# Optimization experiments

Measured on AMD Instinct MI355X. Metric: run time of the kernel, lower is better.

## Reference

```python
import jax, jax.numpy as jnp
import numpy as np
import math

B, LQ, LKV = 8, 1024, 1024
EQ, EKV, H, HD = 1024, 768, 8, 128

def setup_inputs() -> dict:
    key = jax.random.key(0)
    ks = jax.random.split(key, 8)
    def xavier(k, shape, fan_in, fan_out):
        a = math.sqrt(6.0 / (fan_in + fan_out))
        return jax.random.uniform(k, shape, jnp.float32, -a, a)
    return {
        "query": jax.random.normal(ks[0], (B, LQ, EQ), jnp.float32),
        "key": jax.random.normal(ks[1], (B, LKV, EKV), jnp.float32),
        "value": jax.random.normal(ks[2], (B, LKV, EKV), jnp.float32),
        "w_q": xavier(ks[3], (H, EQ, HD), EQ, HD),
        "w_k": xavier(ks[4], (H, EKV, HD), EKV, HD),
        "w_v": xavier(ks[5], (H, EKV, HD), EKV, HD),
        "proj_w": xavier(ks[6], (EQ, H * HD), H * HD, EQ),
        "proj_b": jnp.zeros((EQ,), jnp.float32),
    }

def reference(query, key, value, w_q, w_k, w_v, proj_w, proj_b):
    hd = w_q.shape[-1]
    # per-head projections: [H, B, L, hd]
    q = jnp.einsum('ble,hed->hbld', query, w_q)
    k = jnp.einsum('ble,hed->hbld', key, w_k)
    v = jnp.einsum('ble,hed->hbld', value, w_v)
    # scaled dot-product scores [H, B, Lq, Lkv]
    score = jnp.einsum('hbld,hbmd->hblm', q, k) / jnp.sqrt(jnp.asarray(hd, q.dtype))
    attn = jax.nn.softmax(score, axis=-1)
    out = jnp.einsum('hblm,hbmd->hbld', attn, v)
    # concat heads along feature dim: [B, Lq, H*hd] (head h -> slice h*hd:(h+1)*hd)
    Bsz, Lq = query.shape[0], query.shape[1]
    out = jnp.transpose(out, (1, 2, 0, 3)).reshape(Bsz, Lq, -1)
    out = out @ proj_w.T + proj_b  # dropout is identity at eval
    # torch returns attention_weights as [H*B, Lq, Lkv]
    attn_flat = attn.reshape(-1, attn.shape[-2], attn.shape[-1])
    return out, attn_flat
```

## Files before the change

### kernel.cpp

```cpp
#include <hip/hip_runtime.h>
#include <math.h>


using bf16x8 = __attribute__((ext_vector_type(8))) short;
using f32x4  = __attribute__((ext_vector_type(4))) float;

__device__ __forceinline__ unsigned bf16_rne(float x) {
    unsigned u = __float_as_uint(x);
    return (u + 0x7fffu + ((u >> 16) & 1u)) >> 16;
}

#define AS1 __attribute__((address_space(1)))
#define AS3 __attribute__((address_space(3)))

__device__ __forceinline__ void gl_lds16(const short* g, short* l) {
    __builtin_amdgcn_global_load_lds((AS1 unsigned*)g, (AS3 unsigned*)l, 16, 0, 0);
}

__global__ __launch_bounds__(256) void split_f32(
    const float* __restrict__ src, short* __restrict__ hi,
    short* __restrict__ lo)
{
    const long i = ((long)blockIdx.x * 256 + threadIdx.x) * 8;
    const float4 a = *(const float4*)(src + i);
    const float4 b = *(const float4*)(src + i + 4);
    const float fv[8] = {a.x, a.y, a.z, a.w, b.x, b.y, b.z, b.w};
    bf16x8 h, l;
    #pragma unroll
    for (int j = 0; j < 8; ++j) {
        unsigned hb = bf16_rne(fv[j]);
        h[j] = (short)hb;
        l[j] = (short)bf16_rne(fv[j] - __uint_as_float(hb << 16));
    }
    *(bf16x8*)(hi + i) = h;
    *(bf16x8*)(lo + i) = l;
}

__global__ __launch_bounds__(256) void transpose_split(
    const float* __restrict__ src, short* __restrict__ dhi,
    short* __restrict__ dlo, int R, int C)
{
    __shared__ float tile[32][33];
    src += (long)blockIdx.z * R * C;
    dhi += (long)blockIdx.z * R * C;
    dlo += (long)blockIdx.z * R * C;
    const int r0 = blockIdx.y * 32, c0 = blockIdx.x * 32;
    const int tx = threadIdx.x & 31, ty = threadIdx.x >> 5;
    #pragma unroll
    for (int i = 0; i < 4; ++i)
        tile[ty + i * 8][tx] = src[(long)(r0 + ty + i * 8) * C + c0 + tx];
    __syncthreads();
    #pragma unroll
    for (int i = 0; i < 4; ++i) {
        const float v = tile[tx][ty + i * 8];
        const unsigned h = bf16_rne(v);
        const long o = (long)(c0 + ty + i * 8) * R + r0 + tx;
        dhi[o] = (short)h;
        dlo[o] = (short)bf16_rne(v - __uint_as_float(h << 16));
    }
}

template <bool AF32, int EP, bool BIAS>
__global__ __launch_bounds__(256, 2) void gemm_bb(
    const void* __restrict__ A0, const void* __restrict__ A1, int lda, long aHS, long aBS,
    const short* __restrict__ B0, const short* __restrict__ B1, int ldb, long bHS, long bBS,
    void* __restrict__ C0, void* __restrict__ C1, int ldc, long cHS, long cBS,
    int K, float scale, const float* __restrict__ bias)
{
    const int z = blockIdx.z, hh = z >> 3, bb = z & 7;
    const long aoff = (long)hh * aHS + (long)bb * aBS;
    const long boff = (long)hh * bHS + (long)bb * bBS;
    const long coff = (long)hh * cHS + (long)bb * cBS;

    __shared__ short lAhi[4096];
    __shared__ short lAlo[4096];
    __shared__ short lBhi[4096];
    __shared__ short lBlo[4096];

    const int t    = threadIdx.x;
    const int lane = t & 63, wid = t >> 6;
    const int wr = wid >> 1, wc = wid & 1;
    const int fr = lane & 15, fg = lane >> 4;

    const int m0 = blockIdx.y * 128, n0 = blockIdx.x * 128;

    const short* Bh = B0 + boff;
    const short* Bl = B1 + boff;
    const short* Ah = AF32 ? nullptr : (const short*)A0 + aoff;
    const short* Al = AF32 ? nullptr : (const short*)A1 + aoff;
    const float* Af = AF32 ? (const float*)A0 + aoff : nullptr;

    const int glrow = (lane >> 2);
    const int glk   = (lane & 3) * 8;
    const int srow = t >> 1;
    const int shalf = (t & 1) * 16;

    f32x4 acc[4][4] = {};

    for (int k0 = 0; k0 < K; k0 += 32) {
        if (AF32) {
            const float* g = Af + (long)(m0 + srow) * lda + k0 + shalf;
            const float4 f0 = *(const float4*)(g);
            const float4 f1 = *(const float4*)(g + 4);
            const float4 f2 = *(const float4*)(g + 8);
            const float4 f3 = *(const float4*)(g + 12);
            const float fv[16] = {f0.x, f0.y, f0.z, f0.w, f1.x, f1.y, f1.z, f1.w,
                                  f2.x, f2.y, f2.z, f2.w, f3.x, f3.y, f3.z, f3.w};
            bf16x8 h0, l0, h1, l1;
            #pragma unroll
            for (int i = 0; i < 8; ++i) {
                unsigned ha = bf16_rne(fv[i]);
                h0[i] = (short)ha;
                l0[i] = (short)bf16_rne(fv[i] - __uint_as_float(ha << 16));
                unsigned hb = bf16_rne(fv[8 + i]);
                h1[i] = (short)hb;
                l1[i] = (short)bf16_rne(fv[8 + i] - __uint_as_float(hb << 16));
            }
            const int sb = srow * 32 + shalf;
            *(bf16x8*)&lAhi[sb] = h0;  *(bf16x8*)&lAhi[sb + 8] = h1;
            *(bf16x8*)&lAlo[sb] = l0;  *(bf16x8*)&lAlo[sb + 8] = l1;
        } else {
            #pragma unroll
            for (int j = 0; j < 2; ++j) {
                const int rowb = wid * 32 + j * 16 + glrow;
                const long go = (long)(m0 + rowb) * lda + k0 + glk;
                gl_lds16(Ah + go, &lAhi[(wid * 2 + j) * 512]);
                gl_lds16(Al + go, &lAlo[(wid * 2 + j) * 512]);
            }
        }
        #pragma unroll
        for (int j = 0; j < 2; ++j) {
            const int rowb = wid * 32 + j * 16 + glrow;
            const long go = (long)(n0 + rowb) * ldb + k0 + glk;
            gl_lds16(Bh + go, &lBhi[(wid * 2 + j) * 512]);
            gl_lds16(Bl + go, &lBlo[(wid * 2 + j) * 512]);
        }
        __syncthreads();

        bf16x8 va[4], wa[4];
        #pragma unroll
        for (int m = 0; m < 4; ++m) {
            const int off = (wr * 64 + m * 16 + fr) * 32 + fg * 8;
            va[m] = *(const bf16x8*)&lAhi[off];
            wa[m] = *(const bf16x8*)&lAlo[off];
        }
        #pragma unroll
        for (int n = 0; n < 4; ++n) {
            const int off = (wc * 64 + n * 16 + fr) * 32 + fg * 8;
            const bf16x8 vb = *(const bf16x8*)&lBhi[off];
            const bf16x8 wb = *(const bf16x8*)&lBlo[off];
            #pragma unroll
            for (int m = 0; m < 4; ++m) {
                acc[m][n] = __builtin_amdgcn_mfma_f32_16x16x32_bf16(va[m], vb, acc[m][n], 0, 0, 0);
                acc[m][n] = __builtin_amdgcn_mfma_f32_16x16x32_bf16(va[m], wb, acc[m][n], 0, 0, 0);
                acc[m][n] = __builtin_amdgcn_mfma_f32_16x16x32_bf16(wa[m], vb, acc[m][n], 0, 0, 0);
            }
        }
        __syncthreads();
    }

    #pragma unroll
    for (int m = 0; m < 4; ++m) {
        const int row0 = m0 + wr * 64 + m * 16 + fg * 4;
        #pragma unroll
        for (int n = 0; n < 4; ++n) {
            const int col = n0 + wc * 64 + n * 16 + fr;
            const f32x4 v = acc[m][n];
            if (EP == 0) {
                float* C = (float*)C0 + coff;
                const float bv = BIAS ? bias[col] : 0.0f;
                #pragma unroll
                for (int i = 0; i < 4; ++i)
                    C[(long)(row0 + i) * ldc + col] = v[i] * scale + bv;
            } else if (EP == 1) {
                short* Chp = (short*)C0 + coff;
                short* Clp = (short*)C1 + coff;
                #pragma unroll
                for (int i = 0; i < 4; ++i) {
                    const float val = v[i] * scale;
                    const unsigned h = bf16_rne(val);
                    const long o = (long)(row0 + i) * ldc + col;
                    Chp[o] = (short)h;
                    Clp[o] = (short)bf16_rne(val - __uint_as_float(h << 16));
                }
            } else {
                short* Chp = (short*)C0 + coff;
                short* Clp = (short*)C1 + coff;
                short4 hv, lv;
                const float v0 = v[0] * scale, v1 = v[1] * scale,
                            v2 = v[2] * scale, v3 = v[3] * scale;
                unsigned h;
                h = bf16_rne(v0); hv.x = (short)h; lv.x = (short)bf16_rne(v0 - __uint_as_float(h << 16));
                h = bf16_rne(v1); hv.y = (short)h; lv.y = (short)bf16_rne(v1 - __uint_as_float(h << 16));
                h = bf16_rne(v2); hv.z = (short)h; lv.z = (short)bf16_rne(v2 - __uint_as_float(h << 16));
                h = bf16_rne(v3); hv.w = (short)h; lv.w = (short)bf16_rne(v3 - __uint_as_float(h << 16));
                const long o = (long)col * ldc + row0;
                *(short4*)&Chp[o] = hv;
                *(short4*)&Clp[o] = lv;
            }
        }
    }
}

__global__ __launch_bounds__(256) void softmax_rows(float* __restrict__ attn)
{
    const long row = blockIdx.x;
    float* p = attn + row * 1024 + (long)threadIdx.x * 4;
    float4 v = *reinterpret_cast<float4*>(p);

    float m = fmaxf(fmaxf(v.x, v.y), fmaxf(v.z, v.w));
    #pragma unroll
    for (int off = 32; off > 0; off >>= 1)
        m = fmaxf(m, __shfl_down(m, off));

    __shared__ float red[4];
    const int wave = threadIdx.x >> 6, lane = threadIdx.x & 63;
    if (lane == 0) red[wave] = m;
    __syncthreads();
    m = fmaxf(fmaxf(red[0], red[1]), fmaxf(red[2], red[3]));
    __syncthreads();

    v.x = __expf(v.x - m); v.y = __expf(v.y - m);
    v.z = __expf(v.z - m); v.w = __expf(v.w - m);
    float s = v.x + v.y + v.z + v.w;
    #pragma unroll
    for (int off = 32; off > 0; off >>= 1)
        s += __shfl_down(s, off);
    if (lane == 0) red[wave] = s;
    __syncthreads();
    s = red[0] + red[1] + red[2] + red[3];

    const float r = 1.0f / s;
    v.x *= r; v.y *= r; v.z *= r; v.w *= r;
    *reinterpret_cast<float4*>(p) = v;
}

extern "C" void kernel_launch(void* const* d_in, const int* in_sizes, int n_in,
                              void* d_out, int out_size, void* d_ws, size_t ws_size,
                              hipStream_t stream)
{
    const float* query  = (const float*)d_in[0];
    const float* key    = (const float*)d_in[1];
    const float* value  = (const float*)d_in[2];
    const float* w_q    = (const float*)d_in[3];
    const float* w_k    = (const float*)d_in[4];
    const float* w_v    = (const float*)d_in[5];
    const float* proj_w = (const float*)d_in[6];
    const float* proj_b = (const float*)d_in[7];

    float* out  = (float*)d_out;
    float* attn = out + (size_t)8 * 1024 * 1024;

    short* ws   = (short*)d_ws;
    short* Qhi  = ws;
    short* Qlo  = Qhi + 8388608;
    short* Khi  = Qlo + 8388608;
    short* Klo  = Khi + 8388608;
    short* VThi = Klo + 8388608;
    short* VTlo = VThi + 8388608;
    short* pwh  = VTlo + 8388608;
    short* pwl  = pwh + 1048576;
    short* Ohi  = Qhi;
    short* Olo  = Qlo;

    short* sc   = (short*)attn;
    short* wTqh = sc;
    short* wTql = wTqh + 1048576;
    short* wTkh = wTql + 1048576;
    short* wTkl = wTkh + 786432;
    short* wTvh = wTkl + 786432;
    short* wTvl = wTvh + 786432;
    short* qsh  = wTvl + 786432;
    short* qsl  = qsh + 8388608;
    short* ksh  = qsl + 8388608;
    short* ksl  = ksh + 6291456;
    short* vsh  = ksl + 6291456;
    short* vsl  = vsh + 6291456;

    const dim3 blk(256);
    const float isq = 0.08838834764831845f;

    split_f32<<<4096, blk, 0, stream>>>(query, qsh, qsl);
    split_f32<<<3072, blk, 0, stream>>>(key, ksh, ksl);
    split_f32<<<3072, blk, 0, stream>>>(value, vsh, vsl);
    split_f32<<<512,  blk, 0, stream>>>(proj_w, pwh, pwl);
    transpose_split<<<dim3(4, 32, 8), blk, 0, stream>>>(w_q, wTqh, wTql, 1024, 128);
    transpose_split<<<dim3(4, 24, 8), blk, 0, stream>>>(w_k, wTkh, wTkl, 768, 128);
    transpose_split<<<dim3(4, 24, 8), blk, 0, stream>>>(w_v, wTvh, wTvl, 768, 128);

    gemm_bb<false, 1, false><<<dim3(1, 8, 64), blk, 0, stream>>>(
        qsh, qsl, 1024, 0L, 1048576L,
        wTqh, wTql, 1024, 131072L, 0L,
        Qhi, Qlo, 128, 1048576L, 131072L,
        1024, isq, nullptr);

    gemm_bb<false, 1, false><<<dim3(1, 8, 64), blk, 0, stream>>>(
        ksh, ksl, 768, 0L, 786432L,
        wTkh, wTkl, 768, 98304L, 0L,
        Khi, Klo, 128, 1048576L, 131072L,
        768, 1.0f, nullptr);

    gemm_bb<false, 2, false><<<dim3(1, 8, 64), blk, 0, stream>>>(
        vsh, vsl, 768, 0L, 786432L,
        wTvh, wTvl, 768, 98304L, 0L,
        VThi, VTlo, 1024, 1048576L, 131072L,
        768, 1.0f, nullptr);

    gemm_bb<false, 0, false><<<dim3(8, 8, 64), blk, 0, stream>>>(
        Qhi, Qlo, 128, 1048576L, 131072L,
        Khi, Klo, 128, 1048576L, 131072L,
        attn, nullptr, 1024, 8388608L, 1048576L,
        128, 1.0f, nullptr);

    softmax_rows<<<65536, blk, 0, stream>>>(attn);

    gemm_bb<true, 1, false><<<dim3(1, 8, 64), blk, 0, stream>>>(
        attn, nullptr, 1024, 8388608L, 1048576L,
        VThi, VTlo, 1024, 1048576L, 131072L,
        Ohi, Olo, 1024, 128L, 1048576L,
        1024, 1.0f, nullptr);

    gemm_bb<false, 0, true><<<dim3(8, 64, 1), blk, 0, stream>>>(
        Ohi, Olo, 1024, 0L, 0L,
        pwh, pwl, 1024, 0L, 0L,
        out, nullptr, 1024, 0L, 0L,
        1024, 1.0f, proj_b);
}
```

Baseline: 836.0 us.

## Double-buffer LDS tiles in gemm_bb with manual waitcnt pipelining

Splits the GEMM main loop into stage and compute steps over two LDS buffer sets, so the next K-tile's async global-to-LDS loads are issued before the current tile's MFMAs run. Explicit vmcnt/lgkmcnt waits and raw s_barrier calls replace the per-iteration __syncthreads pair. s_setprio is raised around the MFMA block. LDS use per block doubles to 64KB, which could limit occupancy. The f32-A path still converts its tile synchronously inside stage, so it gets less overlap.

```diff
diff --git a/kernel.cpp b/kernel.cpp
--- a/kernel.cpp
+++ b/kernel.cpp
@@ -72,10 +72,8 @@
     const long boff = (long)hh * bHS + (long)bb * bBS;
     const long coff = (long)hh * cHS + (long)bb * cBS;
 
-    __shared__ short lAhi[4096];
-    __shared__ short lAlo[4096];
-    __shared__ short lBhi[4096];
-    __shared__ short lBlo[4096];
+    __shared__ short lA0h[4096], lA0l[4096], lB0h[4096], lB0l[4096];
+    __shared__ short lA1h[4096], lA1l[4096], lB1h[4096], lB1l[4096];
 
     const int t    = threadIdx.x;
     const int lane = t & 63, wid = t >> 6;
@@ -92,18 +90,25 @@
 
     const int glrow = (lane >> 2);
     const int glk   = (lane & 3) * 8;
-    const int srow = t >> 1;
+    const int srow  = t >> 1;
     const int shalf = (t & 1) * 16;
 
     f32x4 acc[4][4] = {};
 
-    for (int k0 = 0; k0 < K; k0 += 32) {
+    auto stage = [&](short* dAh, short* dAl, short* dBh, short* dBl, int kk) {
         if (AF32) {
-            const float* g = Af + (long)(m0 + srow) * lda + k0 + shalf;
+            const float* g = Af + (long)(m0 + srow) * lda + kk + shalf;
             const float4 f0 = *(const float4*)(g);
             const float4 f1 = *(const float4*)(g + 4);
             const float4 f2 = *(const float4*)(g + 8);
             const float4 f3 = *(const float4*)(g + 12);
+            #pragma unroll
+            for (int j = 0; j < 2; ++j) {
+                const int rowb = wid * 32 + j * 16 + glrow;
+                const long go = (long)(n0 + rowb) * ldb + kk + glk;
+                gl_lds16(Bh + go, &dBh[(wid * 2 + j) * 512]);
+                gl_lds16(Bl + go, &dBl[(wid * 2 + j) * 512]);
+            }
             const float fv[16] = {f0.x, f0.y, f0.z, f0.w, f1.x, f1.y, f1.z, f1.w,
                                   f2.x, f2.y, f2.z, f2.w, f3.x, f3.y, f3.z, f3.w};
             bf16x8 h0, l0, h1, l1;
@@ -117,38 +122,41 @@
                 l1[i] = (short)bf16_rne(fv[8 + i] - __uint_as_float(hb << 16));
             }
             const int sb = srow * 32 + shalf;
-            *(bf16x8*)&lAhi[sb] = h0;  *(bf16x8*)&lAhi[sb + 8] = h1;
-            *(bf16x8*)&lAlo[sb] = l0;  *(bf16x8*)&lAlo[sb + 8] = l1;
+            *(bf16x8*)&dAh[sb] = h0;  *(bf16x8*)&dAh[sb + 8] = h1;
+            *(bf16x8*)&dAl[sb] = l0;  *(bf16x8*)&dAl[sb + 8] = l1;
         } else {
             #pragma unroll
             for (int j = 0; j < 2; ++j) {
                 const int rowb = wid * 32 + j * 16 + glrow;
-                const long go = (long)(m0 + rowb) * lda + k0 + glk;
-                gl_lds16(Ah + go, &lAhi[(wid * 2 + j) * 512]);
-                gl_lds16(Al + go, &lAlo[(wid * 2 + j) * 512]);
-            }
-        }
-        #pragma unroll
-        for (int j = 0; j < 2; ++j) {
-            const int rowb = wid * 32 + j * 16 + glrow;
-            const long go = (long)(n0 + rowb) * ldb + k0 + glk;
-            gl_lds16(Bh + go, &lBhi[(wid * 2 + j) * 512]);
-            gl_lds16(Bl + go, &lBlo[(wid * 2 + j) * 512]);
-        }
-        __syncthreads();
-
+                const long go = (long)(m0 + rowb) * lda + kk + glk;
+                gl_lds16(Ah + go, &dAh[(wid * 2 + j) * 512]);
+                gl_lds16(Al + go, &dAl[(wid * 2 + j) * 512]);
+            }
+            #pragma unroll
+            for (int j = 0; j < 2; ++j) {
+                const int rowb = wid * 32 + j * 16 + glrow;
+                const long go = (long)(n0 + rowb) * ldb + kk + glk;
+                gl_lds16(Bh + go, &dBh[(wid * 2 + j) * 512]);
+                gl_lds16(Bl + go, &dBl[(wid * 2 + j) * 512]);
+            }
+        }
+    };
+
+    auto compute = [&](const short* sAh, const short* sAl,
+                       const short* sBh, const short* sBl) {
         bf16x8 va[4], wa[4];
         #pragma unroll
         for (int m = 0; m < 4; ++m) {
             const int off = (wr * 64 + m * 16 + fr) * 32 + fg * 8;
-            va[m] = *(const bf16x8*)&lAhi[off];
-            wa[m] = *(const bf16x8*)&lAlo[off];
-        }
+            va[m] = *(const bf16x8*)&sAh[off];
+            wa[m] = *(const bf16x8*)&sAl[off];
+        }
+        __builtin_amdgcn_s_setprio(1);
         #pragma unroll
         for (int n = 0; n < 4; ++n) {
             const int off = (wc * 64 + n * 16 + fr) * 32 + fg * 8;
-            const bf16x8 vb = *(const bf16x8*)&lBhi[off];
-            const bf16x8 wb = *(const bf16x8*)&lBlo[off];
+            const bf16x8 vb = *(const bf16x8*)&sBh[off];
+            const bf16x8 wb = *(const bf16x8*)&sBl[off];
             #pragma unroll
             for (int m = 0; m < 4; ++m) {
                 acc[m][n] = __builtin_amdgcn_mfma_f32_16x16x32_bf16(va[m], vb, acc[m][n], 0, 0, 0);
@@ -156,7 +164,30 @@
                 acc[m][n] = __builtin_amdgcn_mfma_f32_16x16x32_bf16(wa[m], vb, acc[m][n], 0, 0, 0);
             }
         }
-        __syncthreads();
+        __builtin_amdgcn_s_setprio(0);
+    };
+
+    stage(lA0h, lA0l, lB0h, lB0l, 0);
+    for (int k0 = 0; k0 < K; k0 += 64) {
+        stage(lA1h, lA1l, lB1h, lB1l, k0 + 32);
+        if (AF32) asm volatile("s_waitcnt vmcnt(4)" ::: "memory");
+        else      asm volatile("s_waitcnt vmcnt(8)" ::: "memory");
+        __builtin_amdgcn_s_barrier();
+        compute(lA0h, lA0l, lB0h, lB0l);
+        asm volatile("s_waitcnt lgkmcnt(0)" ::: "memory");
+        __builtin_amdgcn_s_barrier();
+
+        if (k0 + 64 < K) {
+            stage(lA0h, lA0l, lB0h, lB0l, k0 + 64);
+            if (AF32) asm volatile("s_waitcnt vmcnt(4)" ::: "memory");
+            else      asm volatile("s_waitcnt vmcnt(8)" ::: "memory");
+        } else {
+            asm volatile("s_waitcnt vmcnt(0)" ::: "memory");
+        }
+        __builtin_amdgcn_s_barrier();
+        compute(lA1h, lA1l, lB1h, lB1l);
+        asm volatile("s_waitcnt lgkmcnt(0)" ::: "memory");
+        __builtin_amdgcn_s_barrier();
     }
 
     #pragma unroll
```

After: 830.6 us. Within noise of the previous version (-0.6%).
